# Performance work log

Hardware: AMD Instinct MI355X
Metric: run time of the kernel (lower is better)

Reference implementation:

```python
import jax, jax.numpy as jnp
import numpy as np

DIM = 768
B, N = 8, 2048
TEMPERATURE = 3.0


def setup_inputs() -> dict:
    key = jax.random.key(0)
    ks = jax.random.split(key, 5)
    lim = 1.0 / np.sqrt(DIM)
    x = jax.random.normal(ks[0], (B, N, DIM), dtype=jnp.float32)
    # torch Linear params: weight [out, in], bias [out]
    w_qkv = jax.random.uniform(ks[1], (3 * DIM, DIM), minval=-lim, maxval=lim, dtype=jnp.float32)
    b_qkv = jax.random.uniform(ks[2], (3 * DIM,), minval=-lim, maxval=lim, dtype=jnp.float32)
    w_proj = jax.random.uniform(ks[3], (DIM, DIM), minval=-lim, maxval=lim, dtype=jnp.float32)
    b_proj = jax.random.uniform(ks[4], (DIM,), minval=-lim, maxval=lim, dtype=jnp.float32)
    return {"x": x, "w_qkv": w_qkv, "b_qkv": b_qkv, "w_proj": w_proj, "b_proj": b_proj}


def reference(x, w_qkv, b_qkv, w_proj, b_proj):
    scale = DIM ** (-0.5)
    qkv = jnp.einsum('bnd,ed->bne', x, w_qkv) + b_qkv  # [b, n, 3*dim]
    q, k, v = jnp.split(qkv, 3, axis=-1)
    scores = jnp.einsum('bnd,bmd->bnm', q, k) * scale  # [b, n, n]
    attn = jax.nn.softmax(scores / TEMPERATURE, axis=-1)
    # dropout p=0.0 -> identity
    out = jnp.einsum('bnm,bmd->bnd', attn, v)
    return jnp.einsum('bnd,ed->bne', out, w_proj) + b_proj
```

## Files before the change

kernel.cpp:

```cpp
#include <hip/hip_runtime.h>
#include <hip/hip_bf16.h>
#include <math.h>

#define B_BATCH 8
#define SEQ 2048
#define DIM 768
#define E3 2304

typedef __bf16 bf16x8 __attribute__((ext_vector_type(8)));
typedef float floatx4 __attribute__((ext_vector_type(4)));

__device__ __forceinline__ void load_lds_16B(const __hip_bfloat16* g, __hip_bfloat16* l) {
    __builtin_amdgcn_global_load_lds((const __attribute__((address_space(1))) void*)g,
                                     (__attribute__((address_space(3))) void*)l, 16, 0, 0);
}

template<typename T> __device__ __forceinline__ T to_out(float v);
template<> __device__ __forceinline__ float to_out<float>(float v) { return v; }
template<> __device__ __forceinline__ __hip_bfloat16 to_out<__hip_bfloat16>(float v) { return __float2bfloat16(v); }

__global__ __launch_bounds__(256, 4)
void cvt_f32_bf16(const float* __restrict__ in, __hip_bfloat16* __restrict__ out, long n8)
{
    const long i = (long)blockIdx.x * blockDim.x + threadIdx.x;
    if (i >= n8) return;
    const float4* p = (const float4*)in + i * 2;
    const float4 a = p[0], b = p[1];
    union { uint4 u; __hip_bfloat16 h[8]; } t;
    t.h[0] = __float2bfloat16(a.x); t.h[1] = __float2bfloat16(a.y);
    t.h[2] = __float2bfloat16(a.z); t.h[3] = __float2bfloat16(a.w);
    t.h[4] = __float2bfloat16(b.x); t.h[5] = __float2bfloat16(b.y);
    t.h[6] = __float2bfloat16(b.z); t.h[7] = __float2bfloat16(b.w);
    ((uint4*)out)[i] = t.u;
}

__global__ __launch_bounds__(256, 4)
void transpose64(const __hip_bfloat16* __restrict__ in, long ldi, long si,
                 __hip_bfloat16* __restrict__ out, long ldo, long so)
{
    __shared__ __hip_bfloat16 t[64][65];
    in  += (long)blockIdx.z * si;
    out += (long)blockIdx.z * so;
    const int r0 = blockIdx.x * 64;
    const int c0 = blockIdx.y * 64;
    const int tid = threadIdx.x;
    const int r  = tid >> 3;
    const int c8 = (tid & 7) * 8;
#pragma unroll
    for (int h = 0; h < 2; ++h) {
        const int row = r + h * 32;
        union { uint4 u; __hip_bfloat16 v[8]; } tmp;
        tmp.u = *(const uint4*)(in + (long)(r0 + row) * ldi + c0 + c8);
#pragma unroll
        for (int j = 0; j < 8; ++j) t[row][c8 + j] = tmp.v[j];
    }
    __syncthreads();
#pragma unroll
    for (int h = 0; h < 2; ++h) {
        const int cr = r + h * 32;
        union { uint4 u; __hip_bfloat16 v[8]; } tmp;
#pragma unroll
        for (int j = 0; j < 8; ++j) tmp.v[j] = t[c8 + j][cr];
        *(uint4*)(out + (long)(c0 + cr) * ldo + r0 + c8) = tmp.u;
    }
}

template<typename OutT>
__global__ __launch_bounds__(256, 2)
void gemm128(const __hip_bfloat16* __restrict__ A, long lda, long sA,
             const __hip_bfloat16* __restrict__ Bm, long ldb, long sB,
             OutT* __restrict__ C, long ldc, long sC,
             const float* __restrict__ bias, float scale, int K,
             int MB, int NB)
{
    __shared__ __hip_bfloat16 As[128 * 32];
    __shared__ __hip_bfloat16 Bs[128 * 32];

    const int id    = blockIdx.x;
    const int xcd   = id & 7;
    const int jj    = id >> 3;
    const int pairs = gridDim.x / NB;
    const int ppx   = pairs >> 3;
    const int pair  = xcd * ppx + jj / NB;
    const int nblk  = jj % NB;
    const int zblk  = pair / MB;
    const int mblk  = pair % MB;

    A  += (long)zblk * sA;
    Bm += (long)zblk * sB;
    C  += (long)zblk * sC;

    const int n0   = nblk * 128;
    const int m0   = mblk * 128;
    const int tid  = threadIdx.x;
    const int wave = tid >> 6;
    const int lane = tid & 63;
    const int wm   = (wave & 1) * 64;
    const int wn   = (wave >> 1) * 64;

    const int sr = lane >> 2;
    const int sc = (lane & 3) * 8;

    const int fr = lane & 15;
    const int fk = (lane >> 4) * 8;

    floatx4 acc[4][4] = {};

    for (int k0 = 0; k0 < K; k0 += 32) {
#pragma unroll
        for (int c = 0; c < 2; ++c) {
            const int chunk = wave * 2 + c;
            const int row   = chunk * 16 + sr;
            load_lds_16B(A  + (long)(m0 + row) * lda + (k0 + sc), As + chunk * 512);
            load_lds_16B(Bm + (long)(n0 + row) * ldb + (k0 + sc), Bs + chunk * 512);
        }
        __syncthreads();

        bf16x8 af[4], bfr[4];
#pragma unroll
        for (int i = 0; i < 4; ++i) {
            af[i]  = *(const bf16x8*)(As + (wm + i * 16 + fr) * 32 + fk);
            bfr[i] = *(const bf16x8*)(Bs + (wn + i * 16 + fr) * 32 + fk);
        }
#pragma unroll
        for (int mi = 0; mi < 4; ++mi)
#pragma unroll
            for (int ni = 0; ni < 4; ++ni)
                acc[mi][ni] = __builtin_amdgcn_mfma_f32_16x16x32_bf16(
                    af[mi], bfr[ni], acc[mi][ni], 0, 0, 0);
        __syncthreads();
    }

    const int cr = (lane >> 4) * 4;
    const int cc = lane & 15;
#pragma unroll
    for (int ni = 0; ni < 4; ++ni) {
        const int col = n0 + wn + ni * 16 + cc;
        const float bv = bias ? bias[col] : 0.0f;
#pragma unroll
        for (int mi = 0; mi < 4; ++mi) {
#pragma unroll
            for (int r = 0; r < 4; ++r) {
                const int row = m0 + wm + mi * 16 + cr + r;
                C[(long)row * ldc + col] = to_out<OutT>(acc[mi][ni][r] * scale + bv);
            }
        }
    }
}

__global__ __launch_bounds__(256, 4)
void softmax_rows(__hip_bfloat16* __restrict__ S, long sB)
{
    __hip_bfloat16* row = S + (long)blockIdx.z * sB + (long)blockIdx.x * SEQ;
    const int tid  = threadIdx.x;
    const int wave = tid >> 6;
    const int lane = tid & 63;

    union { uint4 u; __hip_bfloat16 h[8]; } t;
    t.u = *(const uint4*)(row + tid * 8);
    float v[8];
#pragma unroll
    for (int j = 0; j < 8; ++j) v[j] = __bfloat162float(t.h[j]);

    float mx = v[0];
#pragma unroll
    for (int j = 1; j < 8; ++j) mx = fmaxf(mx, v[j]);
    for (int off = 32; off > 0; off >>= 1) mx = fmaxf(mx, __shfl_xor(mx, off, 64));

    __shared__ float redm[4], reds[4];
    if (lane == 0) redm[wave] = mx;
    __syncthreads();
    mx = fmaxf(fmaxf(redm[0], redm[1]), fmaxf(redm[2], redm[3]));

    float e[8], s = 0.f;
#pragma unroll
    for (int j = 0; j < 8; ++j) { e[j] = __expf(v[j] - mx); s += e[j]; }
    for (int off = 32; off > 0; off >>= 1) s += __shfl_xor(s, off, 64);
    if (lane == 0) reds[wave] = s;
    __syncthreads();
    s = reds[0] + reds[1] + reds[2] + reds[3];
    const float inv = 1.f / s;

#pragma unroll
    for (int j = 0; j < 8; ++j) t.h[j] = __float2bfloat16(e[j] * inv);
    *(uint4*)(row + tid * 8) = t.u;
}

extern "C" void kernel_launch(void* const* d_in, const int* in_sizes, int n_in,
                              void* d_out, int out_size, void* d_ws, size_t ws_size,
                              hipStream_t stream)
{
    const float* x     = (const float*)d_in[0];
    const float* w_qkv = (const float*)d_in[1];
    const float* b_qkv = (const float*)d_in[2];
    const float* w_prj = (const float*)d_in[3];
    const float* b_prj = (const float*)d_in[4];
    float* out = (float*)d_out;

    const float alpha = 1.0f / (sqrtf((float)DIM) * 3.0f);

    const size_t XE   = (size_t)B_BATCH * SEQ * DIM;
    const size_t WQE  = (size_t)E3 * DIM;
    const size_t WPE  = (size_t)DIM * DIM;
    const size_t QKVE = (size_t)B_BATCH * SEQ * E3;
    const size_t SE   = (size_t)B_BATCH * SEQ * SEQ;
    const size_t OE   = XE;
    dim3 blk(256);

    const size_t full_bytes = (XE + WQE + WPE + QKVE + SE + OE) * sizeof(__hip_bfloat16);

    if (ws_size >= full_bytes) {
        __hip_bfloat16* xb  = (__hip_bfloat16*)d_ws;
        __hip_bfloat16* wqb = xb + XE;
        __hip_bfloat16* wpb = wqb + WQE;
        __hip_bfloat16* qkv = wpb + WPE;
        __hip_bfloat16* S   = qkv + QKVE;
        __hip_bfloat16* O   = S + SE;
        __hip_bfloat16* Vt  = xb;

        cvt_f32_bf16<<<dim3((XE / 8 + 255) / 256), blk, 0, stream>>>(x, xb, XE / 8);
        cvt_f32_bf16<<<dim3((WQE / 8 + 255) / 256), blk, 0, stream>>>(w_qkv, wqb, WQE / 8);
        cvt_f32_bf16<<<dim3((WPE / 8 + 255) / 256), blk, 0, stream>>>(w_prj, wpb, WPE / 8);

        gemm128<__hip_bfloat16><<<dim3(128 * 18), blk, 0, stream>>>(
            xb, DIM, 0, wqb, DIM, 0, qkv, E3, 0, b_qkv, 1.0f, DIM, 128, 18);
        transpose64<<<dim3(SEQ / 64, DIM / 64, B_BATCH), blk, 0, stream>>>(
            qkv + 2 * DIM, E3, (long)SEQ * E3, Vt, SEQ, (long)DIM * SEQ);
        gemm128<__hip_bfloat16><<<dim3(16 * 16 * B_BATCH), blk, 0, stream>>>(
            qkv, E3, (long)SEQ * E3, qkv + DIM, E3, (long)SEQ * E3,
            S, SEQ, (long)SEQ * SEQ, nullptr, alpha, DIM, 16, 16);
        softmax_rows<<<dim3(SEQ, 1, B_BATCH), blk, 0, stream>>>(S, (long)SEQ * SEQ);
        gemm128<__hip_bfloat16><<<dim3(16 * 6 * B_BATCH), blk, 0, stream>>>(
            S, SEQ, (long)SEQ * SEQ, Vt, SEQ, (long)DIM * SEQ,
            O, DIM, (long)SEQ * DIM, nullptr, 1.0f, SEQ, 16, 6);
        gemm128<float><<<dim3(128 * 6), blk, 0, stream>>>(
            O, DIM, 0, wpb, DIM, 0, out, DIM, 0, b_prj, 1.0f, DIM, 128, 6);
    } else {
        const size_t xE  = (size_t)SEQ * DIM;
        const size_t qE  = (size_t)SEQ * E3;
        const size_t sE1 = (size_t)SEQ * SEQ;
        __hip_bfloat16* wqb = (__hip_bfloat16*)d_ws;
        __hip_bfloat16* wpb = wqb + WQE;
        __hip_bfloat16* xb  = wpb + WPE;
        __hip_bfloat16* qkv = xb + xE;
        __hip_bfloat16* S   = qkv + qE;
        __hip_bfloat16* O   = S + sE1;
        __hip_bfloat16* Vt  = xb;

        cvt_f32_bf16<<<dim3((WQE / 8 + 255) / 256), blk, 0, stream>>>(w_qkv, wqb, WQE / 8);
        cvt_f32_bf16<<<dim3((WPE / 8 + 255) / 256), blk, 0, stream>>>(w_prj, wpb, WPE / 8);

        for (int b = 0; b < B_BATCH; ++b) {
            const float* xf = x + (size_t)b * xE;
            cvt_f32_bf16<<<dim3((xE / 8 + 255) / 256), blk, 0, stream>>>(xf, xb, xE / 8);
            gemm128<__hip_bfloat16><<<dim3(16 * 18), blk, 0, stream>>>(
                xb, DIM, 0, wqb, DIM, 0, qkv, E3, 0, b_qkv, 1.0f, DIM, 16, 18);
            transpose64<<<dim3(SEQ / 64, DIM / 64, 1), blk, 0, stream>>>(
                qkv + 2 * DIM, E3, 0, Vt, SEQ, 0);
            gemm128<__hip_bfloat16><<<dim3(16 * 16), blk, 0, stream>>>(
                qkv, E3, 0, qkv + DIM, E3, 0, S, SEQ, 0, nullptr, alpha, DIM, 16, 16);
            softmax_rows<<<dim3(SEQ, 1, 1), blk, 0, stream>>>(S, 0);
            gemm128<__hip_bfloat16><<<dim3(16 * 6), blk, 0, stream>>>(
                S, SEQ, 0, Vt, SEQ, 0, O, DIM, 0, nullptr, 1.0f, SEQ, 16, 6);
            gemm128<float><<<dim3(16 * 6), blk, 0, stream>>>(
                O, DIM, 0, wpb, DIM, 0, out + (size_t)b * xE, DIM, 0, b_prj, 1.0f, DIM, 16, 6);
        }
    }
}
```

Measured before the change: 395.8 us.

## Fuse softmax into score GEMM exp epilogue and PV GEMM row normalisation

```diff
diff --git a/kernel.cpp b/kernel.cpp
--- a/kernel.cpp
+++ b/kernel.cpp
@@ -65,7 +65,7 @@
     }
 }
 
-template<typename OutT>
+template<typename OutT, int EPI>
 __global__ __launch_bounds__(256, 2)
 void gemm128(const __hip_bfloat16* __restrict__ A, long lda, long sA,
              const __hip_bfloat16* __restrict__ Bm, long ldb, long sB,
@@ -75,6 +75,7 @@
 {
     __shared__ __hip_bfloat16 As[128 * 32];
     __shared__ __hip_bfloat16 Bs[128 * 32];
+    __shared__ float lsum[128];
 
     const int id    = blockIdx.x;
     const int xcd   = id & 7;
@@ -105,6 +106,7 @@
     const int fk = (lane >> 4) * 8;
 
     floatx4 acc[4][4] = {};
+    float rsum[4] = {0.f, 0.f, 0.f, 0.f};
 
     for (int k0 = 0; k0 < K; k0 += 32) {
 #pragma unroll
@@ -122,6 +124,13 @@
             af[i]  = *(const bf16x8*)(As + (wm + i * 16 + fr) * 32 + fk);
             bfr[i] = *(const bf16x8*)(Bs + (wn + i * 16 + fr) * 32 + fk);
         }
+        if constexpr (EPI == 2) {
+#pragma unroll
+            for (int mi = 0; mi < 4; ++mi)
+#pragma unroll
+                for (int j = 0; j < 8; ++j)
+                    rsum[mi] += (float)af[mi][j];
+        }
 #pragma unroll
         for (int mi = 0; mi < 4; ++mi)
 #pragma unroll
@@ -131,59 +140,49 @@
         __syncthreads();
     }
 
+    if constexpr (EPI == 2) {
+#pragma unroll
+        for (int mi = 0; mi < 4; ++mi) {
+            rsum[mi] += __shfl_xor(rsum[mi], 16, 64);
+            rsum[mi] += __shfl_xor(rsum[mi], 32, 64);
+        }
+        if (wave < 2 && (lane >> 4) == 0) {
+#pragma unroll
+            for (int mi = 0; mi < 4; ++mi)
+                lsum[wm + mi * 16 + (lane & 15)] = rsum[mi];
+        }
+        __syncthreads();
+    }
+
     const int cr = (lane >> 4) * 4;
     const int cc = lane & 15;
+
+    float inv[4][4];
+    if constexpr (EPI == 2) {
+#pragma unroll
+        for (int mi = 0; mi < 4; ++mi)
+#pragma unroll
+            for (int r = 0; r < 4; ++r)
+                inv[mi][r] = 1.0f / lsum[wm + mi * 16 + cr + r];
+    }
+
 #pragma unroll
     for (int ni = 0; ni < 4; ++ni) {
         const int col = n0 + wn + ni * 16 + cc;
-        const float bv = bias ? bias[col] : 0.0f;
+        const float bv = (EPI == 0 && bias) ? bias[col] : 0.0f;
 #pragma unroll
         for (int mi = 0; mi < 4; ++mi) {
 #pragma unroll
             for (int r = 0; r < 4; ++r) {
                 const int row = m0 + wm + mi * 16 + cr + r;
-                C[(long)row * ldc + col] = to_out<OutT>(acc[mi][ni][r] * scale + bv);
+                float v = acc[mi][ni][r];
+                if constexpr (EPI == 0)      v = v * scale + bv;
+                else if constexpr (EPI == 1) v = __expf(v * scale);
+                else                         v = v * inv[mi][r];
+                C[(long)row * ldc + col] = to_out<OutT>(v);
             }
         }
     }
-}
-
-__global__ __launch_bounds__(256, 4)
-void softmax_rows(__hip_bfloat16* __restrict__ S, long sB)
-{
-    __hip_bfloat16* row = S + (long)blockIdx.z * sB + (long)blockIdx.x * SEQ;
-    const int tid  = threadIdx.x;
-    const int wave = tid >> 6;
-    const int lane = tid & 63;
-
-    union { uint4 u; __hip_bfloat16 h[8]; } t;
-    t.u = *(const uint4*)(row + tid * 8);
-    float v[8];
-#pragma unroll
-    for (int j = 0; j < 8; ++j) v[j] = __bfloat162float(t.h[j]);
-
-    float mx = v[0];
-#pragma unroll
-    for (int j = 1; j < 8; ++j) mx = fmaxf(mx, v[j]);
-    for (int off = 32; off > 0; off >>= 1) mx = fmaxf(mx, __shfl_xor(mx, off, 64));
-
-    __shared__ float redm[4], reds[4];
-    if (lane == 0) redm[wave] = mx;
-    __syncthreads();
-    mx = fmaxf(fmaxf(redm[0], redm[1]), fmaxf(redm[2], redm[3]));
-
-    float e[8], s = 0.f;
-#pragma unroll
-    for (int j = 0; j < 8; ++j) { e[j] = __expf(v[j] - mx); s += e[j]; }
-    for (int off = 32; off > 0; off >>= 1) s += __shfl_xor(s, off, 64);
-    if (lane == 0) reds[wave] = s;
-    __syncthreads();
-    s = reds[0] + reds[1] + reds[2] + reds[3];
-    const float inv = 1.f / s;
-
-#pragma unroll
-    for (int j = 0; j < 8; ++j) t.h[j] = __float2bfloat16(e[j] * inv);
-    *(uint4*)(row + tid * 8) = t.u;
 }
 
 extern "C" void kernel_launch(void* const* d_in, const int* in_sizes, int n_in,
@@ -222,18 +221,17 @@
         cvt_f32_bf16<<<dim3((WQE / 8 + 255) / 256), blk, 0, stream>>>(w_qkv, wqb, WQE / 8);
         cvt_f32_bf16<<<dim3((WPE / 8 + 255) / 256), blk, 0, stream>>>(w_prj, wpb, WPE / 8);
 
-        gemm128<__hip_bfloat16><<<dim3(128 * 18), blk, 0, stream>>>(
+        gemm128<__hip_bfloat16, 0><<<dim3(128 * 18), blk, 0, stream>>>(
             xb, DIM, 0, wqb, DIM, 0, qkv, E3, 0, b_qkv, 1.0f, DIM, 128, 18);
         transpose64<<<dim3(SEQ / 64, DIM / 64, B_BATCH), blk, 0, stream>>>(
             qkv + 2 * DIM, E3, (long)SEQ * E3, Vt, SEQ, (long)DIM * SEQ);
-        gemm128<__hip_bfloat16><<<dim3(16 * 16 * B_BATCH), blk, 0, stream>>>(
+        gemm128<__hip_bfloat16, 1><<<dim3(16 * 16 * B_BATCH), blk, 0, stream>>>(
             qkv, E3, (long)SEQ * E3, qkv + DIM, E3, (long)SEQ * E3,
             S, SEQ, (long)SEQ * SEQ, nullptr, alpha, DIM, 16, 16);
-        softmax_rows<<<dim3(SEQ, 1, B_BATCH), blk, 0, stream>>>(S, (long)SEQ * SEQ);
-        gemm128<__hip_bfloat16><<<dim3(16 * 6 * B_BATCH), blk, 0, stream>>>(
+        gemm128<__hip_bfloat16, 2><<<dim3(16 * 6 * B_BATCH), blk, 0, stream>>>(
             S, SEQ, (long)SEQ * SEQ, Vt, SEQ, (long)DIM * SEQ,
             O, DIM, (long)SEQ * DIM, nullptr, 1.0f, SEQ, 16, 6);
-        gemm128<float><<<dim3(128 * 6), blk, 0, stream>>>(
+        gemm128<float, 0><<<dim3(128 * 6), blk, 0, stream>>>(
             O, DIM, 0, wpb, DIM, 0, out, DIM, 0, b_prj, 1.0f, DIM, 128, 6);
     } else {
         const size_t xE  = (size_t)SEQ * DIM;
@@ -253,16 +251,15 @@
         for (int b = 0; b < B_BATCH; ++b) {
             const float* xf = x + (size_t)b * xE;
             cvt_f32_bf16<<<dim3((xE / 8 + 255) / 256), blk, 0, stream>>>(xf, xb, xE / 8);
-            gemm128<__hip_bfloat16><<<dim3(16 * 18), blk, 0, stream>>>(
+            gemm128<__hip_bfloat16, 0><<<dim3(16 * 18), blk, 0, stream>>>(
                 xb, DIM, 0, wqb, DIM, 0, qkv, E3, 0, b_qkv, 1.0f, DIM, 16, 18);
             transpose64<<<dim3(SEQ / 64, DIM / 64, 1), blk, 0, stream>>>(
                 qkv + 2 * DIM, E3, 0, Vt, SEQ, 0);
-            gemm128<__hip_bfloat16><<<dim3(16 * 16), blk, 0, stream>>>(
+            gemm128<__hip_bfloat16, 1><<<dim3(16 * 16), blk, 0, stream>>>(
                 qkv, E3, 0, qkv + DIM, E3, 0, S, SEQ, 0, nullptr, alpha, DIM, 16, 16);
-            softmax_rows<<<dim3(SEQ, 1, 1), blk, 0, stream>>>(S, 0);
-            gemm128<__hip_bfloat16><<<dim3(16 * 6), blk, 0, stream>>>(
+            gemm128<__hip_bfloat16, 2><<<dim3(16 * 6), blk, 0, stream>>>(
                 S, SEQ, 0, Vt, SEQ, 0, O, DIM, 0, nullptr, 1.0f, SEQ, 16, 6);
-            gemm128<float><<<dim3(16 * 6), blk, 0, stream>>>(
+            gemm128<float, 0><<<dim3(16 * 6), blk, 0, stream>>>(
                 O, DIM, 0, wpb, DIM, 0, out + (size_t)b * xE, DIM, 0, b_prj, 1.0f, DIM, 16, 6);
         }
     }
```

Result: faster. 373.1 us (-5.7%).
